# Optimization experiments

Hardware: AMD Instinct MI355X
Metric: run time of the kernel (lower is better)

The kernel has to match this reference:

```python
import jax, jax.numpy as jnp
import numpy as np

N_EMBD = 1024
N_HEAD = 16
HEAD_DIM = N_EMBD // N_HEAD


def setup_inputs() -> dict:
    key = jax.random.key(0)
    k1, k2, k3 = jax.random.split(key, 3)
    B, T, C = 2, 2048, N_EMBD
    x = jax.random.normal(k1, (B, T, C), dtype=jnp.float32)
    # torch nn.Linear(n_embd, 3*n_embd): weight [3C, C], bias [3C]
    W = jax.random.normal(k2, (3 * C, C), dtype=jnp.float32) * (1.0 / np.sqrt(C))
    b = jax.random.normal(k3, (3 * C,), dtype=jnp.float32) * 0.01
    return {"x": x, "W": W, "b": b}


def reference(x, W, b):
    B, T, C = x.shape
    H, D = N_HEAD, HEAD_DIM
    qkv = jnp.einsum('btc,oc->bto', x, W) + b          # [B,T,3C]
    q, k, v = jnp.split(qkv, 3, axis=2)
    # [B,H,T,D]
    q = q.reshape(B, T, H, D).transpose(0, 2, 1, 3)
    k = k.reshape(B, T, H, D).transpose(0, 2, 1, 3)
    v = v.reshape(B, T, H, D).transpose(0, 2, 1, 3)
    scale = 1.0 / np.sqrt(D).astype(np.float32)
    scores = jnp.einsum('bhid,bhjd->bhij', q, k) * scale   # [B,H,T,T]
    causal = jnp.tril(jnp.ones((T, T), dtype=bool))
    w = jnp.where(causal, jax.nn.relu(scores), 0.0)        # ReLU, no softmax
    y = jnp.einsum('bhij,bhjd->bhid', w, v)                # [B,H,T,D]
    return y.transpose(0, 2, 1, 3).reshape(B, T, C)
```

## Files before the change

### kernel.cpp

```cpp
#include <hip/hip_runtime.h>

typedef __bf16 bf16;
typedef __bf16 bf16x8 __attribute__((ext_vector_type(8)));
typedef float  f32x4  __attribute__((ext_vector_type(4)));

#define T_SEQ   2048
#define D_HEAD  64
#define NH      16
#define BH      32
#define C_EMB   1024
#define WS_STRIDE (BH * T_SEQ * D_HEAD)
#define XN (4096 * 1024)
#define WN (3072 * 1024)
#define WS_NEEDED ((size_t)(3 * WS_STRIDE + XN + WN) * 2)
#define CVT_GRID 3584

__device__ __forceinline__ bf16x8 cvt8(float4 a, float4 b) {
    bf16x8 r;
    r[0] = (__bf16)a.x; r[1] = (__bf16)a.y; r[2] = (__bf16)a.z; r[3] = (__bf16)a.w;
    r[4] = (__bf16)b.x; r[5] = (__bf16)b.y; r[6] = (__bf16)b.z; r[7] = (__bf16)b.w;
    return r;
}

__device__ __forceinline__ void gl_lds16(const bf16* g, bf16* l) {
    __builtin_amdgcn_global_load_lds(
        (const __attribute__((address_space(1))) unsigned int*)g,
        (__attribute__((address_space(3))) unsigned int*)l,
        16, 0, 0);
}

__device__ __forceinline__ unsigned pack_bf16(float a, float b) {
    union { __bf16 h[2]; unsigned u; } pk;
    pk.h[0] = (__bf16)a; pk.h[1] = (__bf16)b;
    return pk.u;
}

__global__ __launch_bounds__(256) void cvt_bf16(
    const float* __restrict__ x, const float* __restrict__ W,
    bf16* __restrict__ xb, bf16* __restrict__ wb)
{
    const int t = blockIdx.x * 256 + threadIdx.x;
    const float* src; bf16* dst; int base;
    if (t < XN / 8) { src = x; dst = xb; base = t * 8; }
    else           { src = W; dst = wb; base = (t - XN / 8) * 8; }
    float4 a = *(const float4*)(src + base);
    float4 b = *(const float4*)(src + base + 4);
    *(bf16x8*)(dst + base) = cvt8(a, b);
}

#define LDA(d, qi) {                                                          \
    const bf16* abase_ = Sh + (d)*16384 + (qi)*8192 + (wm*64 + l15)*64;       \
    _Pragma("unroll")                                                         \
    for (int ii_ = 0; ii_ < 4; ii_++) {                                       \
        _Pragma("unroll")                                                     \
        for (int dk_ = 0; dk_ < 2; dk_++)                                     \
            aF[ii_][dk_] = *(const bf16x8*)(abase_ + ii_*1024                 \
                                            + (((dk_*4 + l4) ^ k7) * 8));     \
    }                                                                         \
}

#define LDB(d) {                                                              \
    const bf16* bbase_ = Sh + 32768 + (d)*12288 + (wn*48 + l15)*64;           \
    _Pragma("unroll")                                                         \
    for (int jj_ = 0; jj_ < 3; jj_++) {                                       \
        _Pragma("unroll")                                                     \
        for (int dk_ = 0; dk_ < 2; dk_++)                                     \
            bF[jj_][dk_] = *(const bf16x8*)(bbase_ + jj_*1024                 \
                                            + (((dk_*4 + l4) ^ k7) * 8));     \
    }                                                                         \
}

#define STA(d, qi, s, ko) gl_lds16(                                           \
    aSrc + (size_t)((qi)*64 + (s)*128) * 1024 + (ko),                         \
    Sh + (d)*16384 + (qi)*8192 + (s)*4096 + w*512)

#define STB(d, u, ko) gl_lds16(                                               \
    bSrc + (size_t)((u)*64) * 1024 + (ko),                                    \
    Sh + 32768 + (d)*12288 + w*512 + (u)*4096)

#define MMA2(qi, ja, jb) {                                                    \
    __builtin_amdgcn_s_setprio(1);                                            \
    _Pragma("unroll")                                                         \
    for (int dk_ = 0; dk_ < 2; dk_++) {                                       \
        _Pragma("unroll")                                                     \
        for (int ii_ = 0; ii_ < 4; ii_++) {                                   \
            acc[(qi)*4 + ii_][ja] = __builtin_amdgcn_mfma_f32_16x16x32_bf16(  \
                aF[ii_][dk_], bF[ja][dk_], acc[(qi)*4 + ii_][ja], 0, 0, 0);   \
            acc[(qi)*4 + ii_][jb] = __builtin_amdgcn_mfma_f32_16x16x32_bf16(  \
                aF[ii_][dk_], bF[jb][dk_], acc[(qi)*4 + ii_][jb], 0, 0, 0);   \
        }                                                                     \
    }                                                                         \
    __builtin_amdgcn_s_setprio(0);                                            \
}

#define MMA1(qi, ja) {                                                        \
    __builtin_amdgcn_s_setprio(1);                                            \
    _Pragma("unroll")                                                         \
    for (int dk_ = 0; dk_ < 2; dk_++) {                                       \
        _Pragma("unroll")                                                     \
        for (int ii_ = 0; ii_ < 4; ii_++)                                     \
            acc[(qi)*4 + ii_][ja] = __builtin_amdgcn_mfma_f32_16x16x32_bf16(  \
                aF[ii_][dk_], bF[ja][dk_], acc[(qi)*4 + ii_][ja], 0, 0, 0);   \
    }                                                                         \
    __builtin_amdgcn_s_setprio(0);                                            \
}

#define BAR   __builtin_amdgcn_s_barrier()
#define LGKM0 asm volatile("s_waitcnt lgkmcnt(0)" ::: "memory")

#define HALF(d, sk)                                                           \
                                                                      \
    LDA(d, 0) LDB(d)                                                          \
    BAR; LGKM0;                                                               \
    MMA2(0, 0, 1)                                                             \
    BAR;                                                                      \
                                                \
    STB(d, 0, sk); STB(d, 1, sk); STB(d, 2, sk);                              \
    STA(d, 0, 0, sk); STA(d, 0, 1, sk);                                       \
    BAR;                                                                      \
    MMA1(0, 2)                                                                \
    BAR;                                                                      \
                                                                      \
    LDA(d, 1)                                                                 \
    BAR; LGKM0;                                                               \
    MMA2(1, 0, 1)                                                             \
    BAR;                                                                      \
                                                    \
    STA(d, 1, 0, sk); STA(d, 1, 1, sk);                                       \
    BAR;                                                                      \
    MMA1(1, 2)                                                                \
    asm volatile("s_waitcnt vmcnt(7)" ::: "memory");                          \
    BAR;

__global__ __launch_bounds__(512, 2) void qkv_gemm4(
    const bf16* __restrict__ xb, const bf16* __restrict__ wb,
    const float* __restrict__ bias, bf16* __restrict__ ws)
{
    __shared__ bf16 Sh[65536];

    const int tid  = threadIdx.x;
    const int lane = tid & 63;
    const int w    = tid >> 6;
    const int wm   = w >> 2, wn = w & 3;
    const int l15  = lane & 15, l4 = lane >> 4;
    const int k7   = l15 & 7;
    const int l8   = lane >> 3;
    const int csw  = (lane & 7) ^ l8;

    const int swz = (blockIdx.x & 7) * 32 + (blockIdx.x >> 3);
    const int bm  = swz >> 4, bn = swz & 15;

    const bf16* aSrc = xb + (size_t)(bm * 256 + w * 8 + l8) * 1024 + csw * 8;
    const bf16* bSrc = wb + (size_t)(bn * 192 + w * 8 + l8) * 1024 + csw * 8;

    f32x4 acc[8][3];
#pragma unroll
    for (int i = 0; i < 8; i++)
#pragma unroll
        for (int j = 0; j < 3; j++) acc[i][j] = (f32x4){0.f, 0.f, 0.f, 0.f};

    bf16x8 aF[4][2], bF[3][2];

    STA(0,0,0,0);  STA(0,0,1,0);  STA(0,1,0,0);  STA(0,1,1,0);
    STB(0,0,0);    STB(0,1,0);    STB(0,2,0);
    STA(1,0,0,64); STA(1,0,1,64); STA(1,1,0,64); STA(1,1,1,64);
    STB(1,0,64);   STB(1,1,64);   STB(1,2,64);
    asm volatile("s_waitcnt vmcnt(7)" ::: "memory");
    BAR;

    for (int it = 0; it < 8; ++it) {
        const int sk0 = (it < 7 ? (2 * it + 2) : 15) * 64;
        const int sk1 = (it < 7 ? (2 * it + 3) : 15) * 64;
        HALF(0, sk0)
        HALF(1, sk1)
    }
    asm volatile("s_waitcnt vmcnt(0)" ::: "memory");
    BAR;

    float bv[3];
#pragma unroll
    for (int ff = 0; ff < 3; ff++)
        bv[ff] = bias[bn * 192 + wn * 48 + ff * 16 + l15];

    const int bi    = bm >> 3;
    const int tBase = (bm & 7) * 256 + wm * 128;
    bf16* Wl = Sh + w * 8192;
    bf16* vt = ws + 2 * (size_t)WS_STRIDE;

#pragma unroll
    for (int ff = 0; ff < 3; ff++) {
        const int col0 = bn * 192 + wn * 48 + ff * 16;
        const int wch  = col0 >> 10;
        const float qs = (wch == 0) ? 0.125f : 1.0f;
        if (wch < 2) {
#pragma unroll
            for (int i = 0; i < 8; i++)
#pragma unroll
                for (int r = 0; r < 4; r++) {
                    const int lt = i * 16 + l4 * 4 + r;
                    const int dl = l15;
                    Wl[ff * 2048 + lt * 16 + (((dl >> 3) ^ lt) & 1) * 8 + (dl & 7)]
                        = (__bf16)((acc[i][ff][r] + bv[ff]) * qs);
                }
        } else {
#pragma unroll
            for (int i = 0; i < 8; i++)
#pragma unroll
                for (int p = 0; p < 2; p++) {
                    const int lt0 = i * 16 + l4 * 4 + 2 * p;
                    const int ct  = lt0 >> 3;
                    const int dl  = l15;
                    *(unsigned*)&Wl[ff * 2048 + dl * 128
                                    + ((ct ^ dl) & 15) * 8 + (lt0 & 7)]
                        = pack_bf16(acc[i][ff][2 * p] + bv[ff],
                                    acc[i][ff][2 * p + 1] + bv[ff]);
                }
        }
    }
    __syncthreads();

#pragma unroll
    for (int ff = 0; ff < 3; ff++) {
        const int col0 = bn * 192 + wn * 48 + ff * 16;
        const int wch  = col0 >> 10;
        const int cc   = col0 & 1023;
        const int hh   = cc >> 6;
        const int dd0  = cc & 63;
        if (wch < 2) {
#pragma unroll
            for (int it = 0; it < 4; it++) {
                const int lt = it * 32 + (lane >> 1);
                const int c2 = lane & 1;
                bf16x8 v8 = *(const bf16x8*)&Wl[ff * 2048 + lt * 16
                                                + ((c2 ^ lt) & 1) * 8];
                *(bf16x8*)&ws[(size_t)wch * WS_STRIDE
                              + ((size_t)(bi * NH + hh) * T_SEQ + tBase + lt) * D_HEAD
                              + dd0 + c2 * 8] = v8;
            }
        } else {
#pragma unroll
            for (int e = 0; e < 4; e++) {
                const int dl = e * 4 + l4;
                const int ct = l15;
                bf16x8 v8 = *(const bf16x8*)&Wl[ff * 2048 + dl * 128
                                                + ((ct ^ dl) & 15) * 8];
                *(bf16x8*)&vt[((size_t)(bi * NH + hh) * D_HEAD + dd0 + dl) * T_SEQ
                              + tBase + ct * 8] = v8;
            }
        }
    }
}

__global__ __launch_bounds__(256) void qkv_gemm(
    const float* __restrict__ x, const float* __restrict__ W,
    const float* __restrict__ bias, bf16* __restrict__ ws)
{
    __shared__ bf16 As[128 * 40];
    __shared__ bf16 Bs[128 * 40];

    const int tid  = threadIdx.x;
    const int lane = tid & 63;
    const int w    = tid >> 6;
    const int wm   = w >> 1, wn = w & 1;
    const int l15  = lane & 15, l4 = lane >> 4;
    const int bm   = blockIdx.x / 24, bn = blockIdx.x % 24;

    const int srow = tid >> 1;
    const int scol = (tid & 1) * 16;
    const float* xg = x + (size_t)(bm * 128 + srow) * 1024 + scol;
    const float* wg = W + (size_t)(bn * 128 + srow) * 1024 + scol;
    bf16* asw = &As[srow * 40 + scol];
    bf16* bsw = &Bs[srow * 40 + scol];

    f32x4 acc[4][4];
#pragma unroll
    for (int i = 0; i < 4; i++)
#pragma unroll
        for (int j = 0; j < 4; j++) acc[i][j] = (f32x4){0.f, 0.f, 0.f, 0.f};

    float bv[4];
#pragma unroll
    for (int j = 0; j < 4; j++) bv[j] = bias[bn * 128 + wn * 64 + j * 16 + l15];

    for (int kk = 0; kk < 32; ++kk) {
        const float* xp = xg + kk * 32;
        const float* wp = wg + kk * 32;
        float4 a0 = *(const float4*)(xp + 0);
        float4 a1 = *(const float4*)(xp + 4);
        float4 a2 = *(const float4*)(xp + 8);
        float4 a3 = *(const float4*)(xp + 12);
        float4 b0 = *(const float4*)(wp + 0);
        float4 b1 = *(const float4*)(wp + 4);
        float4 b2 = *(const float4*)(wp + 8);
        float4 b3 = *(const float4*)(wp + 12);

        __syncthreads();
        *(bf16x8*)(asw + 0) = cvt8(a0, a1);
        *(bf16x8*)(asw + 8) = cvt8(a2, a3);
        *(bf16x8*)(bsw + 0) = cvt8(b0, b1);
        *(bf16x8*)(bsw + 8) = cvt8(b2, b3);
        __syncthreads();

        bf16x8 aF[4], bF[4];
#pragma unroll
        for (int s = 0; s < 4; s++) {
            aF[s] = *(const bf16x8*)&As[(wm * 64 + s * 16 + l15) * 40 + l4 * 8];
            bF[s] = *(const bf16x8*)&Bs[(wn * 64 + s * 16 + l15) * 40 + l4 * 8];
        }
#pragma unroll
        for (int i = 0; i < 4; i++)
#pragma unroll
            for (int j = 0; j < 4; j++)
                acc[i][j] = __builtin_amdgcn_mfma_f32_16x16x32_bf16(
                    aF[i], bF[j], acc[i][j], 0, 0, 0);
    }

#pragma unroll
    for (int i = 0; i < 4; i++) {
#pragma unroll
        for (int j = 0; j < 4; j++) {
            const int n     = bn * 128 + wn * 64 + j * 16 + l15;
            const int which = n >> 10;
            const int cc    = n & 1023;
            const int h     = cc >> 6, d = cc & 63;
            const float qs  = (which == 0) ? 0.125f : 1.0f;
#pragma unroll
            for (int r = 0; r < 4; r++) {
                const int m  = bm * 128 + wm * 64 + i * 16 + l4 * 4 + r;
                const int bi = m >> 11, t = m & 2047;
                const int bh = bi * NH + h;
                const float v = (acc[i][j][r] + bv[j]) * qs;
                size_t idx;
                if (which == 2)
                    idx = 2 * (size_t)WS_STRIDE + ((size_t)bh * D_HEAD + d) * T_SEQ + t;
                else
                    idx = (size_t)which * WS_STRIDE + ((size_t)bh * T_SEQ + t) * D_HEAD + d;
                ws[idx] = (__bf16)v;
            }
        }
    }
}

#define KSTAGE(jt_, p_) {                                                     \
    _Pragma("unroll")                                                         \
    for (int e_ = 0; e_ < 4; e_++) {                                          \
        const int rb_ = w * 32 + e_ * 8;                                      \
        gl_lds16(kg + (size_t)((jt_) * 128 + rb_ + ksub) * 64                 \
                    + ((kc ^ ksub ^ (e_ << 1)) * 8),                          \
                 &Kb[p_][rb_ * 64]);                                          \
    }                                                                         \
}

#define VSTAGE(jt_) {                                                         \
    _Pragma("unroll")                                                         \
    for (int e_ = 0; e_ < 4; e_++) {                                          \
        const int rb_ = w * 16 + e_ * 4;                                      \
        const int sw_ = (rb_ & 12) + vsub;                 \
        gl_lds16(vt + (size_t)(rb_ + vsub) * T_SEQ + (jt_) * 128              \
                    + ((vc ^ sw_) * 8),                                       \
                 &Vts[rb_ * 128]);                                            \
    }                                                                         \
}

__global__ __launch_bounds__(256) void attn(
    const bf16* __restrict__ ws, float* __restrict__ out)
{
    __shared__ bf16 Kb[2][128 * 64];
    __shared__ bf16 Vts[64 * 128];

    const int tid  = threadIdx.x;
    const int lane = tid & 63;
    const int w    = tid >> 6;
    const int l15  = lane & 15, qd = lane >> 4;

    const int bh = blockIdx.x & 31;
    const int u  = blockIdx.x >> 5;
    const int qt = (u < 8) ? u : (23 - u);
    const int nj = qt + 1;
    const int qb = qt * 128;

    const bf16* qg = ws + (size_t)bh * (T_SEQ * D_HEAD);
    const bf16* kg = ws + WS_STRIDE + (size_t)bh * (T_SEQ * D_HEAD);
    const bf16* vt = ws + 2 * (size_t)WS_STRIDE + (size_t)bh * (D_HEAD * T_SEQ);
    const int b = bh >> 4, h = bh & 15;

    const int ksub = lane >> 3;
    const int kc   = lane & 7;
    const int vsub = qd;
    const int vc   = l15;

    const int krow0 = 8 * (l15 >> 2) + (l15 & 3);
    const int pos00 = qd ^ (l15 & 3) ^ ((l15 >> 2) << 1);
    const int kbO0  = krow0 * 64 + pos00 * 8;
    const int kbO1  = krow0 * 64 + (pos00 ^ 4) * 8;

    bf16x8 qF[2][2];
#pragma unroll
    for (int sm = 0; sm < 2; sm++)
#pragma unroll
        for (int dk = 0; dk < 2; dk++)
            qF[sm][dk] = *(const bf16x8*)(qg
                + (qb + w * 32 + sm * 16 + l15) * 64 + dk * 32 + qd * 8);

    f32x4 o[2][4];
#pragma unroll
    for (int sm = 0; sm < 2; sm++)
#pragma unroll
        for (int sd = 0; sd < 4; sd++) o[sm][sd] = (f32x4){0.f, 0.f, 0.f, 0.f};

    KSTAGE(0, 0);

    for (int jt = 0; jt < nj; ++jt) {
        const int p = jt & 1;
        const bool more = (jt + 1 < nj);
        VSTAGE(jt);
        if (more) {
            KSTAGE(jt + 1, p ^ 1);
            asm volatile("s_waitcnt vmcnt(8)" ::: "memory");
        } else {
            asm volatile("s_waitcnt vmcnt(4)" ::: "memory");
        }
        BAR;

        const bf16* kb0 = &Kb[p][kbO0];
        const bf16* kb1 = &Kb[p][kbO1];

        const bool need_mask = (jt == nj - 1);
        unsigned PK[2][8][2];
#pragma unroll
        for (int m = 0; m < 4; m++) {
            bf16x8 kf[2][2];
            kf[0][0] = *(const bf16x8*)(kb0 + m * 2048);
            kf[0][1] = *(const bf16x8*)(kb1 + m * 2048);
            kf[1][0] = *(const bf16x8*)(kb1 + m * 2048 + 256);
            kf[1][1] = *(const bf16x8*)(kb0 + m * 2048 + 256);
#pragma unroll
            for (int h2 = 0; h2 < 2; h2++) {
                const int kn = 2 * m + h2;
                f32x4 s0 = {0.f, 0.f, 0.f, 0.f}, s1 = {0.f, 0.f, 0.f, 0.f};
                __builtin_amdgcn_s_setprio(1);
                s0 = __builtin_amdgcn_mfma_f32_16x16x32_bf16(kf[h2][0], qF[0][0], s0, 0, 0, 0);
                s0 = __builtin_amdgcn_mfma_f32_16x16x32_bf16(kf[h2][1], qF[0][1], s0, 0, 0, 0);
                s1 = __builtin_amdgcn_mfma_f32_16x16x32_bf16(kf[h2][0], qF[1][0], s1, 0, 0, 0);
                s1 = __builtin_amdgcn_mfma_f32_16x16x32_bf16(kf[h2][1], qF[1][1], s1, 0, 0, 0);
                __builtin_amdgcn_s_setprio(0);
                const int keyb = jt * 128 + 32 * m + 8 * qd + 4 * h2;
#pragma unroll
                for (int sm = 0; sm < 2; sm++) {
                    const f32x4 sv = sm ? s1 : s0;
                    float v[4];
#pragma unroll
                    for (int r = 0; r < 4; r++) v[r] = fmaxf(sv[r], 0.f);
                    if (need_mask) {
                        const int q = qb + w * 32 + sm * 16 + l15;
#pragma unroll
                        for (int r = 0; r < 4; r++)
                            if (q < keyb + r) v[r] = 0.f;
                    }
                    PK[sm][kn][0] = pack_bf16(v[0], v[1]);
                    PK[sm][kn][1] = pack_bf16(v[2], v[3]);
                }
            }
        }

        if (more) asm volatile("s_waitcnt vmcnt(4)" ::: "memory");
        else      asm volatile("s_waitcnt vmcnt(0)" ::: "memory");
        BAR;

#pragma unroll
        for (int kk = 0; kk < 4; kk++) {
            bf16x8 pF[2];
#pragma unroll
            for (int sm = 0; sm < 2; sm++) {
                union { unsigned dw[4]; bf16x8 v; } uu;
                uu.dw[0] = PK[sm][2 * kk + 0][0];
                uu.dw[1] = PK[sm][2 * kk + 0][1];
                uu.dw[2] = PK[sm][2 * kk + 1][0];
                uu.dw[3] = PK[sm][2 * kk + 1][1];
                pF[sm] = uu.v;
            }
            __builtin_amdgcn_s_setprio(1);
#pragma unroll
            for (int sd = 0; sd < 4; sd++) {
                bf16x8 vf = *(const bf16x8*)&Vts[(sd * 16 + l15) * 128
                                                 + (((kk * 4 + qd) ^ l15) * 8)];
                o[0][sd] = __builtin_amdgcn_mfma_f32_16x16x32_bf16(pF[0], vf, o[0][sd], 0, 0, 0);
                o[1][sd] = __builtin_amdgcn_mfma_f32_16x16x32_bf16(pF[1], vf, o[1][sd], 0, 0, 0);
            }
            __builtin_amdgcn_s_setprio(0);
        }

        BAR;
    }

#pragma unroll
    for (int sm = 0; sm < 2; sm++)
#pragma unroll
        for (int sd = 0; sd < 4; sd++) {
            const int d = sd * 16 + l15;
#pragma unroll
            for (int r = 0; r < 4; r++) {
                const int t = qb + w * 32 + sm * 16 + qd * 4 + r;
                out[((size_t)b * T_SEQ + t) * C_EMB + h * 64 + d] = o[sm][sd][r];
            }
        }
}

extern "C" void kernel_launch(void* const* d_in, const int* in_sizes, int n_in,
                              void* d_out, int out_size, void* d_ws, size_t ws_size,
                              hipStream_t stream) {
    const float* x    = (const float*)d_in[0];
    const float* W    = (const float*)d_in[1];
    const float* bias = (const float*)d_in[2];
    float* out        = (float*)d_out;
    bf16*  ws         = (bf16*)d_ws;

    if (ws_size >= WS_NEEDED) {
        bf16* xb = ws + 3 * (size_t)WS_STRIDE;
        bf16* wb = xb + XN;
        cvt_bf16<<<dim3(CVT_GRID), dim3(256), 0, stream>>>(x, W, xb, wb);
        qkv_gemm4<<<dim3(256), dim3(512), 0, stream>>>(xb, wb, bias, ws);
    } else {
        qkv_gemm<<<dim3(768), dim3(256), 0, stream>>>(x, W, bias, ws);
    }
    attn<<<dim3(512), dim3(256), 0, stream>>>(ws, out);
}
```

Baseline: 146.9 us.

## Replace LDS-staged attention with single-wave blocks loading K/V directly into registers

```diff
diff --git a/kernel.cpp b/kernel.cpp
--- a/kernel.cpp
+++ b/kernel.cpp
@@ -341,41 +341,37 @@
     }
 }
 
-#define KSTAGE(jt_, p_) {                                                     \
-    _Pragma("unroll")                                                         \
-    for (int e_ = 0; e_ < 4; e_++) {                                          \
-        const int rb_ = w * 32 + e_ * 8;                                      \
-        gl_lds16(kg + (size_t)((jt_) * 128 + rb_ + ksub) * 64                 \
-                    + ((kc ^ ksub ^ (e_ << 1)) * 8),                          \
-                 &Kb[p_][rb_ * 64]);                                          \
-    }                                                                         \
-}
-
-#define VSTAGE(jt_) {                                                         \
-    _Pragma("unroll")                                                         \
-    for (int e_ = 0; e_ < 4; e_++) {                                          \
-        const int rb_ = w * 16 + e_ * 4;                                      \
-        const int sw_ = (rb_ & 12) + vsub;                 \
-        gl_lds16(vt + (size_t)(rb_ + vsub) * T_SEQ + (jt_) * 128              \
-                    + ((vc ^ sw_) * 8),                                       \
-                 &Vts[rb_ * 128]);                                            \
-    }                                                                         \
-}
-
-__global__ __launch_bounds__(256) void attn(
+#define KLOAD(jt_) {                                                          \
+    const bf16* kb_ = kg + (size_t)(jt_) * 8192 + kOff;                       \
+    _Pragma("unroll")                                                         \
+    for (int m_ = 0; m_ < 4; m_++)                                            \
+        _Pragma("unroll")                                                     \
+        for (int h_ = 0; h_ < 2; h_++)                                        \
+            _Pragma("unroll")                                                 \
+            for (int d_ = 0; d_ < 2; d_++)                                    \
+                kA[m_][h_][d_] = *(const bf16x8*)(kb_ + m_ * 2048             \
+                                                  + h_ * 256 + d_ * 32);      \
+}
+
+#define VLOAD(jt_) {                                                          \
+    const bf16* vb_ = vt + vOff + (jt_) * 128;                                \
+    _Pragma("unroll")                                                         \
+    for (int s_ = 0; s_ < 4; s_++)                                            \
+        _Pragma("unroll")                                                     \
+        for (int k_ = 0; k_ < 4; k_++)                                        \
+            vv[s_][k_] = *(const bf16x8*)(vb_ + s_ * 32768 + k_ * 32);        \
+}
+
+__global__ __launch_bounds__(64) void attn(
     const bf16* __restrict__ ws, float* __restrict__ out)
 {
-    __shared__ bf16 Kb[2][128 * 64];
-    __shared__ bf16 Vts[64 * 128];
-
-    const int tid  = threadIdx.x;
-    const int lane = tid & 63;
-    const int w    = tid >> 6;
+    const int lane = threadIdx.x & 63;
     const int l15  = lane & 15, qd = lane >> 4;
 
     const int bh = blockIdx.x & 31;
     const int u  = blockIdx.x >> 5;
-    const int qt = (u < 8) ? u : (23 - u);
+    const int qt = 15 - (u & 15);
+    const int rg = u >> 4;
     const int nj = qt + 1;
     const int qb = qt * 128;
 
@@ -384,15 +380,8 @@
     const bf16* vt = ws + 2 * (size_t)WS_STRIDE + (size_t)bh * (D_HEAD * T_SEQ);
     const int b = bh >> 4, h = bh & 15;
 
-    const int ksub = lane >> 3;
-    const int kc   = lane & 7;
-    const int vsub = qd;
-    const int vc   = l15;
-
-    const int krow0 = 8 * (l15 >> 2) + (l15 & 3);
-    const int pos00 = qd ^ (l15 & 3) ^ ((l15 >> 2) << 1);
-    const int kbO0  = krow0 * 64 + pos00 * 8;
-    const int kbO1  = krow0 * 64 + (pos00 ^ 4) * 8;
+    const int kOff = (8 * (l15 >> 2) + (l15 & 3)) * 64 + qd * 8;
+    const int vOff = l15 * 2048 + qd * 8;
 
     bf16x8 qF[2][2];
 #pragma unroll
@@ -400,7 +389,7 @@
 #pragma unroll
         for (int dk = 0; dk < 2; dk++)
             qF[sm][dk] = *(const bf16x8*)(qg
-                + (qb + w * 32 + sm * 16 + l15) * 64 + dk * 32 + qd * 8);
+                + (qb + rg * 32 + sm * 16 + l15) * 64 + dk * 32 + qd * 8);
 
     f32x4 o[2][4];
 #pragma unroll
@@ -408,43 +397,29 @@
 #pragma unroll
         for (int sd = 0; sd < 4; sd++) o[sm][sd] = (f32x4){0.f, 0.f, 0.f, 0.f};
 
-    KSTAGE(0, 0);
+    bf16x8 kA[4][2][2];
+    bf16x8 vv[4][4];
+
+    KLOAD(0);
 
     for (int jt = 0; jt < nj; ++jt) {
-        const int p = jt & 1;
-        const bool more = (jt + 1 < nj);
-        VSTAGE(jt);
-        if (more) {
-            KSTAGE(jt + 1, p ^ 1);
-            asm volatile("s_waitcnt vmcnt(8)" ::: "memory");
-        } else {
-            asm volatile("s_waitcnt vmcnt(4)" ::: "memory");
-        }
-        BAR;
-
-        const bf16* kb0 = &Kb[p][kbO0];
-        const bf16* kb1 = &Kb[p][kbO1];
+        VLOAD(jt);
 
         const bool need_mask = (jt == nj - 1);
         unsigned PK[2][8][2];
 #pragma unroll
         for (int m = 0; m < 4; m++) {
-            bf16x8 kf[2][2];
-            kf[0][0] = *(const bf16x8*)(kb0 + m * 2048);
-            kf[0][1] = *(const bf16x8*)(kb1 + m * 2048);
-            kf[1][0] = *(const bf16x8*)(kb1 + m * 2048 + 256);
-            kf[1][1] = *(const bf16x8*)(kb0 + m * 2048 + 256);
 #pragma unroll
             for (int h2 = 0; h2 < 2; h2++) {
-                const int kn = 2 * m + h2;
                 f32x4 s0 = {0.f, 0.f, 0.f, 0.f}, s1 = {0.f, 0.f, 0.f, 0.f};
                 __builtin_amdgcn_s_setprio(1);
-                s0 = __builtin_amdgcn_mfma_f32_16x16x32_bf16(kf[h2][0], qF[0][0], s0, 0, 0, 0);
-                s0 = __builtin_amdgcn_mfma_f32_16x16x32_bf16(kf[h2][1], qF[0][1], s0, 0, 0, 0);
-                s1 = __builtin_amdgcn_mfma_f32_16x16x32_bf16(kf[h2][0], qF[1][0], s1, 0, 0, 0);
-                s1 = __builtin_amdgcn_mfma_f32_16x16x32_bf16(kf[h2][1], qF[1][1], s1, 0, 0, 0);
+                s0 = __builtin_amdgcn_mfma_f32_16x16x32_bf16(kA[m][h2][0], qF[0][0], s0, 0, 0, 0);
+                s0 = __builtin_amdgcn_mfma_f32_16x16x32_bf16(kA[m][h2][1], qF[0][1], s0, 0, 0, 0);
+                s1 = __builtin_amdgcn_mfma_f32_16x16x32_bf16(kA[m][h2][0], qF[1][0], s1, 0, 0, 0);
+                s1 = __builtin_amdgcn_mfma_f32_16x16x32_bf16(kA[m][h2][1], qF[1][1], s1, 0, 0, 0);
                 __builtin_amdgcn_s_setprio(0);
                 const int keyb = jt * 128 + 32 * m + 8 * qd + 4 * h2;
+                const int kn = 2 * m + h2;
 #pragma unroll
                 for (int sm = 0; sm < 2; sm++) {
                     const f32x4 sv = sm ? s1 : s0;
@@ -452,7 +427,7 @@
 #pragma unroll
                     for (int r = 0; r < 4; r++) v[r] = fmaxf(sv[r], 0.f);
                     if (need_mask) {
-                        const int q = qb + w * 32 + sm * 16 + l15;
+                        const int q = qb + rg * 32 + sm * 16 + l15;
 #pragma unroll
                         for (int r = 0; r < 4; r++)
                             if (q < keyb + r) v[r] = 0.f;
@@ -463,9 +438,7 @@
             }
         }
 
-        if (more) asm volatile("s_waitcnt vmcnt(4)" ::: "memory");
-        else      asm volatile("s_waitcnt vmcnt(0)" ::: "memory");
-        BAR;
+        if (jt + 1 < nj) KLOAD(jt + 1);
 
 #pragma unroll
         for (int kk = 0; kk < 4; kk++) {
@@ -482,15 +455,11 @@
             __builtin_amdgcn_s_setprio(1);
 #pragma unroll
             for (int sd = 0; sd < 4; sd++) {
-                bf16x8 vf = *(const bf16x8*)&Vts[(sd * 16 + l15) * 128
-                                                 + (((kk * 4 + qd) ^ l15) * 8)];
-                o[0][sd] = __builtin_amdgcn_mfma_f32_16x16x32_bf16(pF[0], vf, o[0][sd], 0, 0, 0);
-                o[1][sd] = __builtin_amdgcn_mfma_f32_16x16x32_bf16(pF[1], vf, o[1][sd], 0, 0, 0);
+                o[0][sd] = __builtin_amdgcn_mfma_f32_16x16x32_bf16(pF[0], vv[sd][kk], o[0][sd], 0, 0, 0);
+                o[1][sd] = __builtin_amdgcn_mfma_f32_16x16x32_bf16(pF[1], vv[sd][kk], o[1][sd], 0, 0, 0);
             }
             __builtin_amdgcn_s_setprio(0);
         }
-
-        BAR;
     }
 
 #pragma unroll
@@ -500,7 +469,7 @@
             const int d = sd * 16 + l15;
 #pragma unroll
             for (int r = 0; r < 4; r++) {
-                const int t = qb + w * 32 + sm * 16 + qd * 4 + r;
+                const int t = qb + rg * 32 + sm * 16 + qd * 4 + r;
                 out[((size_t)b * T_SEQ + t) * C_EMB + h * 64 + d] = o[sm][sd][r];
             }
         }
@@ -523,5 +492,5 @@
     } else {
         qkv_gemm<<<dim3(768), dim3(256), 0, stream>>>(x, W, bias, ws);
     }
-    attn<<<dim3(512), dim3(256), 0, stream>>>(ws, out);
-}
+    attn<<<dim3(2048), dim3(64), 0, stream>>>(ws, out);
+}
```

New measurement: 185.4 us. +26.2%, slower.

## Halve attention query tile to 64 rows and skip fully masked key subtiles

Applied to the files above, without the earlier changes.

```diff
diff --git a/kernel.cpp b/kernel.cpp
--- a/kernel.cpp
+++ b/kernel.cpp
@@ -375,9 +375,11 @@
 
     const int bh = blockIdx.x & 31;
     const int u  = blockIdx.x >> 5;
-    const int qt = (u < 8) ? u : (23 - u);
+    const int s  = 31 - u;
+    const int qt = s >> 1;
+    const int hs = s & 1;
     const int nj = qt + 1;
-    const int qb = qt * 128;
+    const int qb = s * 64;
 
     const bf16* qg = ws + (size_t)bh * (T_SEQ * D_HEAD);
     const bf16* kg = ws + WS_STRIDE + (size_t)bh * (T_SEQ * D_HEAD);
@@ -394,19 +396,15 @@
     const int kbO0  = krow0 * 64 + pos00 * 8;
     const int kbO1  = krow0 * 64 + (pos00 ^ 4) * 8;
 
-    bf16x8 qF[2][2];
-#pragma unroll
-    for (int sm = 0; sm < 2; sm++)
-#pragma unroll
-        for (int dk = 0; dk < 2; dk++)
-            qF[sm][dk] = *(const bf16x8*)(qg
-                + (qb + w * 32 + sm * 16 + l15) * 64 + dk * 32 + qd * 8);
-
-    f32x4 o[2][4];
-#pragma unroll
-    for (int sm = 0; sm < 2; sm++)
-#pragma unroll
-        for (int sd = 0; sd < 4; sd++) o[sm][sd] = (f32x4){0.f, 0.f, 0.f, 0.f};
+    bf16x8 qF[2];
+#pragma unroll
+    for (int dk = 0; dk < 2; dk++)
+        qF[dk] = *(const bf16x8*)(qg
+            + (qb + w * 16 + l15) * 64 + dk * 32 + qd * 8);
+
+    f32x4 o[4];
+#pragma unroll
+    for (int sd = 0; sd < 4; sd++) o[sd] = (f32x4){0.f, 0.f, 0.f, 0.f};
 
     KSTAGE(0, 0);
 
@@ -426,39 +424,36 @@
         const bf16* kb1 = &Kb[p][kbO1];
 
         const bool need_mask = (jt == nj - 1);
-        unsigned PK[2][8][2];
+        const int mMax = (need_mask && hs == 0) ? 2 : 4;
+        unsigned PK[8][2];
 #pragma unroll
         for (int m = 0; m < 4; m++) {
-            bf16x8 kf[2][2];
-            kf[0][0] = *(const bf16x8*)(kb0 + m * 2048);
-            kf[0][1] = *(const bf16x8*)(kb1 + m * 2048);
-            kf[1][0] = *(const bf16x8*)(kb1 + m * 2048 + 256);
-            kf[1][1] = *(const bf16x8*)(kb0 + m * 2048 + 256);
-#pragma unroll
-            for (int h2 = 0; h2 < 2; h2++) {
-                const int kn = 2 * m + h2;
-                f32x4 s0 = {0.f, 0.f, 0.f, 0.f}, s1 = {0.f, 0.f, 0.f, 0.f};
-                __builtin_amdgcn_s_setprio(1);
-                s0 = __builtin_amdgcn_mfma_f32_16x16x32_bf16(kf[h2][0], qF[0][0], s0, 0, 0, 0);
-                s0 = __builtin_amdgcn_mfma_f32_16x16x32_bf16(kf[h2][1], qF[0][1], s0, 0, 0, 0);
-                s1 = __builtin_amdgcn_mfma_f32_16x16x32_bf16(kf[h2][0], qF[1][0], s1, 0, 0, 0);
-                s1 = __builtin_amdgcn_mfma_f32_16x16x32_bf16(kf[h2][1], qF[1][1], s1, 0, 0, 0);
-                __builtin_amdgcn_s_setprio(0);
-                const int keyb = jt * 128 + 32 * m + 8 * qd + 4 * h2;
-#pragma unroll
-                for (int sm = 0; sm < 2; sm++) {
-                    const f32x4 sv = sm ? s1 : s0;
+            if (m < mMax) {
+                bf16x8 kf[2][2];
+                kf[0][0] = *(const bf16x8*)(kb0 + m * 2048);
+                kf[0][1] = *(const bf16x8*)(kb1 + m * 2048);
+                kf[1][0] = *(const bf16x8*)(kb1 + m * 2048 + 256);
+                kf[1][1] = *(const bf16x8*)(kb0 + m * 2048 + 256);
+#pragma unroll
+                for (int h2 = 0; h2 < 2; h2++) {
+                    const int kn = 2 * m + h2;
+                    f32x4 s0 = {0.f, 0.f, 0.f, 0.f};
+                    __builtin_amdgcn_s_setprio(1);
+                    s0 = __builtin_amdgcn_mfma_f32_16x16x32_bf16(kf[h2][0], qF[0], s0, 0, 0, 0);
+                    s0 = __builtin_amdgcn_mfma_f32_16x16x32_bf16(kf[h2][1], qF[1], s0, 0, 0, 0);
+                    __builtin_amdgcn_s_setprio(0);
+                    const int keyb = jt * 128 + 32 * m + 8 * qd + 4 * h2;
                     float v[4];
 #pragma unroll
-                    for (int r = 0; r < 4; r++) v[r] = fmaxf(sv[r], 0.f);
+                    for (int r = 0; r < 4; r++) v[r] = fmaxf(s0[r], 0.f);
                     if (need_mask) {
-                        const int q = qb + w * 32 + sm * 16 + l15;
+                        const int q = qb + w * 16 + l15;
 #pragma unroll
                         for (int r = 0; r < 4; r++)
                             if (q < keyb + r) v[r] = 0.f;
                     }
-                    PK[sm][kn][0] = pack_bf16(v[0], v[1]);
-                    PK[sm][kn][1] = pack_bf16(v[2], v[3]);
+                    PK[kn][0] = pack_bf16(v[0], v[1]);
+                    PK[kn][1] = pack_bf16(v[2], v[3]);
                 }
             }
         }
@@ -469,41 +464,36 @@
 
 #pragma unroll
         for (int kk = 0; kk < 4; kk++) {
-            bf16x8 pF[2];
-#pragma unroll
-            for (int sm = 0; sm < 2; sm++) {
+            if (kk < mMax) {
                 union { unsigned dw[4]; bf16x8 v; } uu;
-                uu.dw[0] = PK[sm][2 * kk + 0][0];
-                uu.dw[1] = PK[sm][2 * kk + 0][1];
-                uu.dw[2] = PK[sm][2 * kk + 1][0];
-                uu.dw[3] = PK[sm][2 * kk + 1][1];
-                pF[sm] = uu.v;
+                uu.dw[0] = PK[2 * kk + 0][0];
+                uu.dw[1] = PK[2 * kk + 0][1];
+                uu.dw[2] = PK[2 * kk + 1][0];
+                uu.dw[3] = PK[2 * kk + 1][1];
+                const bf16x8 pF = uu.v;
+                __builtin_amdgcn_s_setprio(1);
+#pragma unroll
+                for (int sd = 0; sd < 4; sd++) {
+                    bf16x8 vf = *(const bf16x8*)&Vts[(sd * 16 + l15) * 128
+                                                     + (((kk * 4 + qd) ^ l15) * 8)];
+                    o[sd] = __builtin_amdgcn_mfma_f32_16x16x32_bf16(pF, vf, o[sd], 0, 0, 0);
+                }
+                __builtin_amdgcn_s_setprio(0);
             }
-            __builtin_amdgcn_s_setprio(1);
-#pragma unroll
-            for (int sd = 0; sd < 4; sd++) {
-                bf16x8 vf = *(const bf16x8*)&Vts[(sd * 16 + l15) * 128
-                                                 + (((kk * 4 + qd) ^ l15) * 8)];
-                o[0][sd] = __builtin_amdgcn_mfma_f32_16x16x32_bf16(pF[0], vf, o[0][sd], 0, 0, 0);
-                o[1][sd] = __builtin_amdgcn_mfma_f32_16x16x32_bf16(pF[1], vf, o[1][sd], 0, 0, 0);
-            }
-            __builtin_amdgcn_s_setprio(0);
         }
 
         BAR;
     }
 
 #pragma unroll
-    for (int sm = 0; sm < 2; sm++)
-#pragma unroll
-        for (int sd = 0; sd < 4; sd++) {
-            const int d = sd * 16 + l15;
-#pragma unroll
-            for (int r = 0; r < 4; r++) {
-                const int t = qb + w * 32 + sm * 16 + qd * 4 + r;
-                out[((size_t)b * T_SEQ + t) * C_EMB + h * 64 + d] = o[sm][sd][r];
-            }
-        }
+    for (int sd = 0; sd < 4; sd++) {
+        const int d = sd * 16 + l15;
+#pragma unroll
+        for (int r = 0; r < 4; r++) {
+            const int t = qb + w * 16 + qd * 4 + r;
+            out[((size_t)b * T_SEQ + t) * C_EMB + h * 64 + d] = o[sd][r];
+        }
+    }
 }
 
 extern "C" void kernel_launch(void* const* d_in, const int* in_sizes, int n_in,
@@ -523,5 +513,5 @@
     } else {
         qkv_gemm<<<dim3(768), dim3(256), 0, stream>>>(x, W, bias, ws);
     }
-    attn<<<dim3(512), dim3(256), 0, stream>>>(ws, out);
-}
+    attn<<<dim3(1024), dim3(256), 0, stream>>>(ws, out);
+}
```

Result: faster. 140.1 us (-4.6%).
